# Kernel tuning notes

Hardware: AMD Instinct MI355X
Metric: run time of the kernel (lower is better)

The kernel has to match this reference:

```python
import jax, jax.numpy as jnp
import numpy as np

L, H, P = 16384, 256, 512


def setup_inputs() -> dict:
    key = jax.random.key(0)
    ks = jax.random.split(key, 7)
    return {
        "input_sequence": jax.random.normal(ks[0], (L, H), jnp.float32),
        "A_diag": jax.random.normal(ks[1], (P,), jnp.float32) * 2.0,
        "G_diag": jax.random.uniform(ks[2], (P,), jnp.float32),  # in [0,1): keeps 1 - sigmoid(dt)*G > 0
        "dt": jax.random.normal(ks[3], (P,), jnp.float32) * 0.5,
        "B": jax.random.uniform(ks[4], (P, H, 2), jnp.float32, -1.0, 1.0) / np.sqrt(H).astype(np.float32),
        "C": jax.random.uniform(ks[5], (H, P, 2), jnp.float32, -1.0, 1.0) / np.sqrt(P).astype(np.float32),
        "D": jax.random.normal(ks[6], (H,), jnp.float32),
    }


def _combine(q_i, q_j):
    # q = (A, b); A: (..., 4, P) real 2x2 block-diagonal entries [A,B,C,D], b: (..., 2, P) complex
    A_i, b_i = q_i
    A_j, b_j = q_j
    iA, iB, iC, iD = A_i[..., 0, :], A_i[..., 1, :], A_i[..., 2, :], A_i[..., 3, :]
    jA, jB, jC, jD = A_j[..., 0, :], A_j[..., 1, :], A_j[..., 2, :], A_j[..., 3, :]
    A_new = jnp.stack(
        [jA * iA + jB * iC, jA * iB + jB * iD, jC * iA + jD * iC, jC * iB + jD * iD],
        axis=-2,
    )
    b1, b2 = b_i[..., 0, :], b_i[..., 1, :]
    b_new = jnp.stack([jA * b1 + jB * b2, jC * b1 + jD * b2], axis=-2) + b_j
    return (A_new, b_new)


def reference(input_sequence, A_diag, G_diag, dt, B, C, D):
    # complex parameter assembly
    B_c = B[..., 0] + 1j * B[..., 1]      # (P, H) complex
    C_c = C[..., 0] + 1j * C[..., 1]      # (H, P) complex

    # _soft_project_AGdt
    dts = jax.nn.sigmoid(dt)
    G = jax.nn.relu(G_diag)
    root = jnp.sqrt(1.0 - dts * G)
    denom = jnp.maximum(dts ** 2, 1e-6)
    A_low = (2.0 - dts * G - 2.0 * root) / denom
    A_high = (2.0 - dts * G + 2.0 * root) / denom
    A = A_low + jax.nn.relu(A_diag - A_low) - jax.nn.relu(A_diag - A_high)

    # Bu_k = B_complex @ u_k for all k: (L, P) complex64
    Bu = input_sequence.astype(B_c.dtype) @ B_c.T

    # IMEX2 transition matrix (diagonal 2x2 blocks), constant over time
    M = jnp.stack(
        [1.0 - dts * G, -dts * A, dts * (1.0 - dts * G), 1.0 - dts ** 2 * A],
        axis=0,
    )  # (4, P)
    seq_len = input_sequence.shape[0]
    M_el = jnp.broadcast_to(M, (seq_len, 4, M.shape[-1]))          # (L, 4, P)
    F = jnp.stack([dts * Bu, dts ** 2 * Bu], axis=1)               # (L, 2, P) complex

    _, xs = jax.lax.associative_scan(_combine, (M_el, F))
    ys = xs[:, 1, :]                                                # x-component, (L, P) complex

    out = (ys @ C_c.T).real.astype(input_sequence.dtype) + input_sequence * D
    return out
```

## Files before the change

kernel.cpp:

```cpp
#include <hip/hip_runtime.h>
#include <math.h>

#define L_SEQ 16384
#define H_DIM 256
#define P_DIM 512
#define CL 64
#define NC (L_SEQ / CL)

typedef __attribute__((ext_vector_type(8))) short bf16x8;
typedef __attribute__((ext_vector_type(4))) float f32x4;

static __device__ __forceinline__ unsigned short f2bf(float f) {
  unsigned int u = __builtin_bit_cast(unsigned int, f);
  u += 0x7FFFu + ((u >> 16) & 1u);
  return (unsigned short)(u >> 16);
}
static __device__ __forceinline__ float bflo(unsigned int v) {
  return __builtin_bit_cast(float, v << 16);
}
static __device__ __forceinline__ float bfhi(unsigned int v) {
  return __builtin_bit_cast(float, v & 0xFFFF0000u);
}

__global__ __launch_bounds__(256) void prep_all(
    const float* __restrict__ A_diag, const float* __restrict__ G_diag,
    const float* __restrict__ dt, const float* __restrict__ B,
    const float* __restrict__ C, const float* __restrict__ u,
    float* __restrict__ prm, unsigned short* __restrict__ W1b,
    unsigned short* __restrict__ W2b, unsigned short* __restrict__ ub) {
  const int b = blockIdx.x;
  const int t = threadIdx.x;
  if (b < 2) {
    int p = b * 256 + t;
    float dts = 1.0f / (1.0f + expf(-dt[p]));
    float G = fmaxf(G_diag[p], 0.0f);
    float g = dts * G;
    float root = sqrtf(1.0f - g);
    float denom = fmaxf(dts * dts, 1e-6f);
    float A_low  = (2.0f - g - 2.0f * root) / denom;
    float A_high = (2.0f - g + 2.0f * root) / denom;
    float Ad = A_diag[p];
    float A = A_low + fmaxf(Ad - A_low, 0.0f) - fmaxf(Ad - A_high, 0.0f);
    float m00 = 1.0f - g;
    float m01 = -dts * A;
    float m10 = dts * (1.0f - g);
    float m11 = 1.0f - dts * dts * A;
    float c00 = m00, c01 = m01, c10 = m10, c11 = m11;
#pragma unroll
    for (int i = 0; i < 6; i++) {
      float n00 = c00 * c00 + c01 * c10;
      float n01 = c00 * c01 + c01 * c11;
      float n10 = c10 * c00 + c11 * c10;
      float n11 = c10 * c01 + c11 * c11;
      c00 = n00; c01 = n01; c10 = n10; c11 = n11;
    }
    prm[0 * P_DIM + p] = m00;
    prm[1 * P_DIM + p] = m01;
    prm[2 * P_DIM + p] = m10;
    prm[3 * P_DIM + p] = m11;
    prm[4 * P_DIM + p] = dts;
    prm[5 * P_DIM + p] = dts * dts;
    prm[6 * P_DIM + p] = c00;
    prm[7 * P_DIM + p] = c01;
    prm[8 * P_DIM + p] = c10;
    prm[9 * P_DIM + p] = c11;
  } else if (b < 2 + 1024) {
    int idx = (b - 2) * 256 + t;
    int n = idx >> 8;
    int k = idx & 255;
    int p = n >> 1, c = n & 1;
    W1b[idx] = f2bf(B[(p * H_DIM + k) * 2 + c]);
  } else if (b < 2 + 2048) {
    int idx = (b - 1026) * 256 + t;
    int h = idx >> 10;
    int k = idx & 1023;
    int p = k >> 1, c = k & 1;
    float v = C[(h * P_DIM + p) * 2 + c];
    W2b[idx] = f2bf(c ? -v : v);
  } else {
    int idx = (b - 2050) * 256 + t;
    float4 v = ((const float4*)u)[idx];
    ushort4 o;
    o.x = f2bf(v.x); o.y = f2bf(v.y); o.z = f2bf(v.z); o.w = f2bf(v.w);
    ((ushort4*)ub)[idx] = o;
  }
}

template <int BM, int BN, bool OUT_BF16, bool EPI>
__global__ __launch_bounds__(256) void gemm_mfma(
    const unsigned short* __restrict__ A, const unsigned short* __restrict__ W,
    void* __restrict__ OutV, int M, int N, int K,
    const float* __restrict__ U, const float* __restrict__ Dv) {
  constexpr int WR = BM / 2;
  constexpr int MR = WR / 16;
  constexpr int WC = BN / 2;
  constexpr int NF = WC / 16;
  __shared__ unsigned short tA[BM * 32];
  __shared__ unsigned short tW[BN * 32];
  const int tid = threadIdx.x;
  const int lane = tid & 63;
  const int wid = tid >> 6;
  const int wr = wid >> 1;
  const int wc = wid & 1;
  const int bm = blockIdx.x * BM;
  const int bn = blockIdx.y * BN;

  f32x4 acc[MR][NF] = {};

  const int srow = lane >> 2;
  const int soff = (lane & 3) * 8;

  for (int k0 = 0; k0 < K; k0 += 32) {
    __syncthreads();
#pragma unroll
    for (int c = wid; c < BM / 16; c += 4) {
      const unsigned short* src = A + (size_t)(bm + c * 16 + srow) * K + k0 + soff;
      __builtin_amdgcn_global_load_lds(
          (const __attribute__((address_space(1))) void*)src,
          (__attribute__((address_space(3))) void*)(tA + c * 512), 16, 0, 0);
    }
#pragma unroll
    for (int c = wid; c < BN / 16; c += 4) {
      const unsigned short* src = W + (size_t)(bn + c * 16 + srow) * K + k0 + soff;
      __builtin_amdgcn_global_load_lds(
          (const __attribute__((address_space(1))) void*)src,
          (__attribute__((address_space(3))) void*)(tW + c * 512), 16, 0, 0);
    }
    __syncthreads();

    const int rA = lane & 15;
    const int kc = (lane >> 4) * 8;
    bf16x8 af[MR], wf[NF];
#pragma unroll
    for (int i = 0; i < MR; i++)
      af[i] = *(const bf16x8*)&tA[(wr * WR + i * 16 + rA) * 32 + kc];
#pragma unroll
    for (int j = 0; j < NF; j++)
      wf[j] = *(const bf16x8*)&tW[(wc * WC + j * 16 + rA) * 32 + kc];
#pragma unroll
    for (int i = 0; i < MR; i++)
#pragma unroll
      for (int j = 0; j < NF; j++)
        acc[i][j] = __builtin_amdgcn_mfma_f32_16x16x32_bf16(af[i], wf[j], acc[i][j], 0, 0, 0);
  }

  const int cr = (lane >> 4) * 4;
  const int cc = lane & 15;
#pragma unroll
  for (int i = 0; i < MR; i++) {
#pragma unroll
    for (int j = 0; j < NF; j++) {
      const int row0 = bm + wr * WR + i * 16 + cr;
      const int col = bn + wc * WC + j * 16 + cc;
#pragma unroll
      for (int q = 0; q < 4; q++) {
        float v = acc[i][j][q];
        size_t idx = (size_t)(row0 + q) * N + col;
        if (OUT_BF16) {
          ((unsigned short*)OutV)[idx] = f2bf(v);
        } else {
          if (EPI) v = fmaf(U[idx], Dv[col], v);
          ((float*)OutV)[idx] = v;
        }
      }
    }
  }
}

__global__ __launch_bounds__(256) void scan_local(
    const unsigned int* __restrict__ Bu16, const float* __restrict__ prm,
    float4* __restrict__ finals) {
  int tid = blockIdx.x * 256 + threadIdx.x;
  int p = tid & (P_DIM - 1);
  int c = tid >> 9;
  float m00 = prm[0 * P_DIM + p], m01 = prm[1 * P_DIM + p];
  float m10 = prm[2 * P_DIM + p], m11 = prm[3 * P_DIM + p];
  float dts = prm[4 * P_DIM + p], dts2 = prm[5 * P_DIM + p];
  float x1r = 0.f, x2r = 0.f, x1i = 0.f, x2i = 0.f;
  const unsigned int* src = Bu16 + (size_t)c * CL * P_DIM + p;
#pragma unroll 8
  for (int i = 0; i < CL; i++) {
    unsigned int v = src[(size_t)i * P_DIM];
    float bx = bflo(v), by = bfhi(v);
    float n1r = fmaf(m00, x1r, fmaf(m01, x2r, dts * bx));
    float n2r = fmaf(m10, x1r, fmaf(m11, x2r, dts2 * bx));
    float n1i = fmaf(m00, x1i, fmaf(m01, x2i, dts * by));
    float n2i = fmaf(m10, x1i, fmaf(m11, x2i, dts2 * by));
    x1r = n1r; x2r = n2r; x1i = n1i; x2i = n2i;
  }
  finals[c * P_DIM + p] = make_float4(x1r, x2r, x1i, x2i);
}

__global__ __launch_bounds__(NC) void scan_carry(
    const float4* __restrict__ finals, const float* __restrict__ prm,
    float4* __restrict__ carry) {
  int p = blockIdx.x;
  int c = threadIdx.x;
  __shared__ float4 sb[NC];
  float m00 = prm[6 * P_DIM + p], m01 = prm[7 * P_DIM + p];
  float m10 = prm[8 * P_DIM + p], m11 = prm[9 * P_DIM + p];
  float4 b = finals[c * P_DIM + p];
  for (int o = 1; o < NC; o <<= 1) {
    sb[c] = b;
    __syncthreads();
    float4 nb = (c >= o) ? sb[c - o] : make_float4(0.f, 0.f, 0.f, 0.f);
    __syncthreads();
    b.x = fmaf(m00, nb.x, fmaf(m01, nb.y, b.x));
    b.y = fmaf(m10, nb.x, fmaf(m11, nb.y, b.y));
    b.z = fmaf(m00, nb.z, fmaf(m01, nb.w, b.z));
    b.w = fmaf(m10, nb.z, fmaf(m11, nb.w, b.w));
    float n00 = m00 * m00 + m01 * m10;
    float n01 = m00 * m01 + m01 * m11;
    float n10 = m10 * m00 + m11 * m10;
    float n11 = m10 * m01 + m11 * m11;
    m00 = n00; m01 = n01; m10 = n10; m11 = n11;
  }
  if (c + 1 < NC) carry[(c + 1) * P_DIM + p] = b;
  if (c == 0) carry[p] = make_float4(0.f, 0.f, 0.f, 0.f);
}

__global__ __launch_bounds__(256) void scan_final(
    unsigned int* __restrict__ Bu16, const float* __restrict__ prm,
    const float4* __restrict__ carry) {
  int tid = blockIdx.x * 256 + threadIdx.x;
  int p = tid & (P_DIM - 1);
  int c = tid >> 9;
  float m00 = prm[0 * P_DIM + p], m01 = prm[1 * P_DIM + p];
  float m10 = prm[2 * P_DIM + p], m11 = prm[3 * P_DIM + p];
  float dts = prm[4 * P_DIM + p], dts2 = prm[5 * P_DIM + p];
  float4 s = carry[c * P_DIM + p];
  float x1r = s.x, x2r = s.y, x1i = s.z, x2i = s.w;
  unsigned int* src = Bu16 + (size_t)c * CL * P_DIM + p;
#pragma unroll 8
  for (int i = 0; i < CL; i++) {
    unsigned int v = src[(size_t)i * P_DIM];
    float bx = bflo(v), by = bfhi(v);
    float n1r = fmaf(m00, x1r, fmaf(m01, x2r, dts * bx));
    float n2r = fmaf(m10, x1r, fmaf(m11, x2r, dts2 * bx));
    float n1i = fmaf(m00, x1i, fmaf(m01, x2i, dts * by));
    float n2i = fmaf(m10, x1i, fmaf(m11, x2i, dts2 * by));
    src[(size_t)i * P_DIM] = (unsigned int)f2bf(n2r) | ((unsigned int)f2bf(n2i) << 16);
    x1r = n1r; x2r = n2r; x1i = n1i; x2i = n2i;
  }
}

extern "C" void kernel_launch(void* const* d_in, const int* in_sizes, int n_in,
                              void* d_out, int out_size, void* d_ws, size_t ws_size,
                              hipStream_t stream) {
  const float* u      = (const float*)d_in[0];
  const float* A_diag = (const float*)d_in[1];
  const float* G_diag = (const float*)d_in[2];
  const float* dt     = (const float*)d_in[3];
  const float* B      = (const float*)d_in[4];
  const float* C      = (const float*)d_in[5];
  const float* D      = (const float*)d_in[6];
  float* out = (float*)d_out;

  char* w = (char*)d_ws;
  unsigned short* Bu16 = (unsigned short*)w;
  unsigned short* ub   = (unsigned short*)(w + (size_t)L_SEQ * 1024 * 2);
  unsigned short* W1b  = ub + (size_t)L_SEQ * H_DIM;
  unsigned short* W2b  = W1b + 1024 * H_DIM;
  float* prm    = (float*)(W2b + H_DIM * 1024);
  float* finals = prm + 8192;
  float* carryb = finals + (size_t)NC * P_DIM * 4;

  prep_all<<<2 + 1024 + 1024 + 4096, 256, 0, stream>>>(
      A_diag, G_diag, dt, B, C, u, prm, W1b, W2b, ub);

  gemm_mfma<128, 128, true, false><<<dim3(L_SEQ / 128, 1024 / 128), 256, 0, stream>>>(
      ub, W1b, Bu16, L_SEQ, 1024, H_DIM, nullptr, nullptr);

  scan_local<<<(NC * P_DIM) / 256, 256, 0, stream>>>(
      (const unsigned int*)Bu16, prm, (float4*)finals);
  scan_carry<<<P_DIM, NC, 0, stream>>>(
      (const float4*)finals, prm, (float4*)carryb);
  scan_final<<<(NC * P_DIM) / 256, 256, 0, stream>>>(
      (unsigned int*)Bu16, prm, (const float4*)carryb);

  gemm_mfma<32, 256, false, true><<<dim3(L_SEQ / 32, 1), 256, 0, stream>>>(
      Bu16, W2b, out, L_SEQ, H_DIM, 1024, u, D);
}
```

Measured before the change: 83.50 us.

## Fuse final scan pass into output GEMM via LDS-resident chunk states

```diff
diff --git a/kernel.cpp b/kernel.cpp
--- a/kernel.cpp
+++ b/kernel.cpp
@@ -4,7 +4,7 @@
 #define L_SEQ 16384
 #define H_DIM 256
 #define P_DIM 512
-#define CL 64
+#define CL 32
 #define NC (L_SEQ / CL)
 
 typedef __attribute__((ext_vector_type(8))) short bf16x8;
@@ -20,6 +20,9 @@
 }
 static __device__ __forceinline__ float bfhi(unsigned int v) {
   return __builtin_bit_cast(float, v & 0xFFFF0000u);
+}
+static __device__ __forceinline__ float bf2f(unsigned short s) {
+  return __builtin_bit_cast(float, (unsigned int)s << 16);
 }
 
 __global__ __launch_bounds__(256) void prep_all(
@@ -47,7 +50,7 @@
     float m11 = 1.0f - dts * dts * A;
     float c00 = m00, c01 = m01, c10 = m10, c11 = m11;
 #pragma unroll
-    for (int i = 0; i < 6; i++) {
+    for (int i = 0; i < 5; i++) {
       float n00 = c00 * c00 + c01 * c10;
       float n01 = c00 * c01 + c01 * c11;
       float n10 = c10 * c00 + c11 * c10;
@@ -86,11 +89,10 @@
   }
 }
 
-template <int BM, int BN, bool OUT_BF16, bool EPI>
+template <int BM, int BN>
 __global__ __launch_bounds__(256) void gemm_mfma(
     const unsigned short* __restrict__ A, const unsigned short* __restrict__ W,
-    void* __restrict__ OutV, int M, int N, int K,
-    const float* __restrict__ U, const float* __restrict__ Dv) {
+    unsigned short* __restrict__ Out, int M, int N, int K) {
   constexpr int WR = BM / 2;
   constexpr int MR = WR / 16;
   constexpr int WC = BN / 2;
@@ -147,24 +149,15 @@
   const int cr = (lane >> 4) * 4;
   const int cc = lane & 15;
 #pragma unroll
-  for (int i = 0; i < MR; i++) {
+  for (int i = 0; i < MR; i++)
 #pragma unroll
     for (int j = 0; j < NF; j++) {
       const int row0 = bm + wr * WR + i * 16 + cr;
       const int col = bn + wc * WC + j * 16 + cc;
 #pragma unroll
-      for (int q = 0; q < 4; q++) {
-        float v = acc[i][j][q];
-        size_t idx = (size_t)(row0 + q) * N + col;
-        if (OUT_BF16) {
-          ((unsigned short*)OutV)[idx] = f2bf(v);
-        } else {
-          if (EPI) v = fmaf(U[idx], Dv[col], v);
-          ((float*)OutV)[idx] = v;
-        }
-      }
-    }
-  }
+      for (int q = 0; q < 4; q++)
+        Out[(size_t)(row0 + q) * N + col] = f2bf(acc[i][j][q]);
+    }
 }
 
 __global__ __launch_bounds__(256) void scan_local(
@@ -219,28 +212,82 @@
   if (c == 0) carry[p] = make_float4(0.f, 0.f, 0.f, 0.f);
 }
 
-__global__ __launch_bounds__(256) void scan_final(
-    unsigned int* __restrict__ Bu16, const float* __restrict__ prm,
-    const float4* __restrict__ carry) {
-  int tid = blockIdx.x * 256 + threadIdx.x;
-  int p = tid & (P_DIM - 1);
-  int c = tid >> 9;
-  float m00 = prm[0 * P_DIM + p], m01 = prm[1 * P_DIM + p];
-  float m10 = prm[2 * P_DIM + p], m11 = prm[3 * P_DIM + p];
-  float dts = prm[4 * P_DIM + p], dts2 = prm[5 * P_DIM + p];
-  float4 s = carry[c * P_DIM + p];
-  float x1r = s.x, x2r = s.y, x1i = s.z, x2i = s.w;
-  unsigned int* src = Bu16 + (size_t)c * CL * P_DIM + p;
+__global__ __launch_bounds__(256) void gemm2_fused(
+    const unsigned int* __restrict__ Bu16, const float* __restrict__ prm,
+    const float4* __restrict__ carry, const unsigned short* __restrict__ W2b,
+    const unsigned short* __restrict__ ub, const float* __restrict__ Dv,
+    float* __restrict__ out) {
+  __shared__ unsigned int yA[32 * 512];
+  __shared__ unsigned short tW[256 * 32];
+  const int tid = threadIdx.x;
+  const int lane = tid & 63;
+  const int wid = tid >> 6;
+  const int row0 = blockIdx.x * 32;
+
+#pragma unroll
+  for (int h = 0; h < 2; h++) {
+    const int p = tid + h * 256;
+    float m00 = prm[0 * P_DIM + p], m01 = prm[1 * P_DIM + p];
+    float m10 = prm[2 * P_DIM + p], m11 = prm[3 * P_DIM + p];
+    float dts = prm[4 * P_DIM + p], dts2 = prm[5 * P_DIM + p];
+    float4 s = carry[(size_t)blockIdx.x * P_DIM + p];
+    float x1r = s.x, x2r = s.y, x1i = s.z, x2i = s.w;
+    const unsigned int* src = Bu16 + (size_t)row0 * P_DIM + p;
 #pragma unroll 8
-  for (int i = 0; i < CL; i++) {
-    unsigned int v = src[(size_t)i * P_DIM];
-    float bx = bflo(v), by = bfhi(v);
-    float n1r = fmaf(m00, x1r, fmaf(m01, x2r, dts * bx));
-    float n2r = fmaf(m10, x1r, fmaf(m11, x2r, dts2 * bx));
-    float n1i = fmaf(m00, x1i, fmaf(m01, x2i, dts * by));
-    float n2i = fmaf(m10, x1i, fmaf(m11, x2i, dts2 * by));
-    src[(size_t)i * P_DIM] = (unsigned int)f2bf(n2r) | ((unsigned int)f2bf(n2i) << 16);
-    x1r = n1r; x2r = n2r; x1i = n1i; x2i = n2i;
+    for (int i = 0; i < 32; i++) {
+      unsigned int v = src[(size_t)i * P_DIM];
+      float bx = bflo(v), by = bfhi(v);
+      float n1r = fmaf(m00, x1r, fmaf(m01, x2r, dts * bx));
+      float n2r = fmaf(m10, x1r, fmaf(m11, x2r, dts2 * bx));
+      float n1i = fmaf(m00, x1i, fmaf(m01, x2i, dts * by));
+      float n2i = fmaf(m10, x1i, fmaf(m11, x2i, dts2 * by));
+      yA[(i * 512 + p) ^ ((i & 7) << 2)] =
+          (unsigned int)f2bf(n2r) | ((unsigned int)f2bf(n2i) << 16);
+      x1r = n1r; x2r = n2r; x1i = n1i; x2i = n2i;
+    }
+  }
+
+  const int srow = lane >> 2;
+  const int soff = (lane & 3) * 8;
+  const int wr = wid >> 1;
+  const int wc = wid & 1;
+  const int rA = lane & 15;
+  const int kc = (lane >> 4) * 8;
+  const int arow = wr * 16 + rA;
+  const unsigned short* yAs = (const unsigned short*)yA;
+  f32x4 acc[8] = {};
+
+  for (int k0 = 0; k0 < 1024; k0 += 32) {
+    __syncthreads();
+#pragma unroll
+    for (int c = wid; c < 16; c += 4) {
+      const unsigned short* src = W2b + (size_t)(c * 16 + srow) * 1024 + k0 + soff;
+      __builtin_amdgcn_global_load_lds(
+          (const __attribute__((address_space(1))) void*)src,
+          (__attribute__((address_space(3))) void*)(tW + c * 512), 16, 0, 0);
+    }
+    __syncthreads();
+
+    bf16x8 af = *(const bf16x8*)&yAs[((size_t)arow * 1024 + k0 + kc) ^ ((arow & 7) << 3)];
+#pragma unroll
+    for (int j = 0; j < 8; j++) {
+      bf16x8 wf = *(const bf16x8*)&tW[(wc * 128 + j * 16 + rA) * 32 + kc];
+      acc[j] = __builtin_amdgcn_mfma_f32_16x16x32_bf16(af, wf, acc[j], 0, 0, 0);
+    }
+  }
+
+  const int cr = (lane >> 4) * 4;
+  const int cc = lane & 15;
+#pragma unroll
+  for (int j = 0; j < 8; j++) {
+    const int col = wc * 128 + j * 16 + cc;
+    const float d = Dv[col];
+#pragma unroll
+    for (int q = 0; q < 4; q++) {
+      const int row = row0 + wr * 16 + cr + q;
+      const size_t idx = (size_t)row * H_DIM + col;
+      out[idx] = fmaf(bf2f(ub[idx]), d, acc[j][q]);
+    }
   }
 }
 
@@ -268,16 +315,14 @@
   prep_all<<<2 + 1024 + 1024 + 4096, 256, 0, stream>>>(
       A_diag, G_diag, dt, B, C, u, prm, W1b, W2b, ub);
 
-  gemm_mfma<128, 128, true, false><<<dim3(L_SEQ / 128, 1024 / 128), 256, 0, stream>>>(
-      ub, W1b, Bu16, L_SEQ, 1024, H_DIM, nullptr, nullptr);
+  gemm_mfma<128, 128><<<dim3(L_SEQ / 128, 1024 / 128), 256, 0, stream>>>(
+      ub, W1b, Bu16, L_SEQ, 1024, H_DIM);
 
   scan_local<<<(NC * P_DIM) / 256, 256, 0, stream>>>(
       (const unsigned int*)Bu16, prm, (float4*)finals);
   scan_carry<<<P_DIM, NC, 0, stream>>>(
       (const float4*)finals, prm, (float4*)carryb);
-  scan_final<<<(NC * P_DIM) / 256, 256, 0, stream>>>(
-      (unsigned int*)Bu16, prm, (const float4*)carryb);
-
-  gemm_mfma<32, 256, false, true><<<dim3(L_SEQ / 32, 1), 256, 0, stream>>>(
-      Bu16, W2b, out, L_SEQ, H_DIM, 1024, u, D);
-}
+
+  gemm2_fused<<<L_SEQ / 32, 256, 0, stream>>>(
+      (const unsigned int*)Bu16, prm, (const float4*)carryb, W2b, ub, D, out);
+}
```

Measured after the change: 79.54 us. -4.7%, faster.
